# Kernel optimization log

Hardware: AMD Instinct MI355X
Metric: run time of the kernel (lower is better)

## Reference

```python
import jax, jax.numpy as jnp
import numpy as np

B, S, D_IN, D_OUT, H = 2, 2048, 1024, 1024, 16
DH = D_OUT // H

def setup_inputs() -> dict:
    key = jax.random.key(0)
    ks = jax.random.split(key, 6)
    sc = 0.02
    return {
        'x': jax.random.normal(ks[0], (B, S, D_IN), dtype=jnp.float32),
        'Wq': jax.random.normal(ks[1], (D_IN, D_OUT), dtype=jnp.float32) * sc,
        'Wk': jax.random.normal(ks[2], (D_IN, D_OUT), dtype=jnp.float32) * sc,
        'Wv': jax.random.normal(ks[3], (D_IN, D_OUT), dtype=jnp.float32) * sc,
        'Wo': jax.random.normal(ks[4], (D_OUT, D_OUT), dtype=jnp.float32) * sc,
        'bo': jax.random.normal(ks[5], (D_OUT,), dtype=jnp.float32) * sc,
    }

def reference(x, Wq, Wk, Wv, Wo, bo):
    b, s, _ = x.shape
    # projections, split heads: (b, h, s, dh)
    q = (x @ Wq).reshape(b, s, H, DH).transpose(0, 2, 1, 3)
    k = (x @ Wk).reshape(b, s, H, DH).transpose(0, 2, 1, 3)
    v = (x @ Wv).reshape(b, s, H, DH).transpose(0, 2, 1, 3)
    scores = jnp.einsum('bhqd,bhkd->bhqk', q, k)
    causal = jnp.triu(jnp.ones((s, s), dtype=bool), k=1)
    scores = jnp.where(causal, -jnp.inf, scores)
    attn = jax.nn.softmax(scores / jnp.sqrt(jnp.float32(DH)), axis=-1)
    ctx = jnp.einsum('bhqk,bhkd->bhqd', attn, v)
    ctx = ctx.transpose(0, 2, 1, 3).reshape(b, s, D_OUT)
    return ctx @ Wo + bo
```

## Files before the change

kernel.cpp:

```cpp
#include <hip/hip_runtime.h>
#include <hip/hip_bf16.h>
#include <cstdint>

typedef __attribute__((ext_vector_type(8))) __bf16 bf16x8;
typedef __attribute__((ext_vector_type(4))) float f32x4;
typedef __attribute__((ext_vector_type(8))) unsigned short u16x8;
typedef __attribute__((ext_vector_type(4))) unsigned short u16x4;
typedef __attribute__((ext_vector_type(4))) unsigned int u32x4;

#define NEG_INF (-__builtin_inff())

__device__ __forceinline__ unsigned short f2bf(float f) {
    unsigned int u = __builtin_bit_cast(unsigned int, f);
    u += 0x7FFFu + ((u >> 16) & 1u);
    return (unsigned short)(u >> 16);
}
__device__ __forceinline__ float bf2f(unsigned short u) {
    return __builtin_bit_cast(float, (unsigned int)u << 16);
}

__device__ __forceinline__ void gload16(const void* g, void* l) {
    __builtin_amdgcn_global_load_lds(
        (__attribute__((address_space(1))) void*)(uintptr_t)g,
        (__attribute__((address_space(3))) void*)(uint32_t)(uintptr_t)l, 16, 0, 0);
}

__global__ void cast_x_kernel(const float* __restrict__ x, unsigned short* __restrict__ xb) {
    size_t i = (size_t)blockIdx.x * 256 + threadIdx.x;
    const float4* p = (const float4*)x + i * 2;
    float4 a = p[0], c = p[1];
    u16x8 o;
    o[0] = f2bf(a.x); o[1] = f2bf(a.y); o[2] = f2bf(a.z); o[3] = f2bf(a.w);
    o[4] = f2bf(c.x); o[5] = f2bf(c.y); o[6] = f2bf(c.z); o[7] = f2bf(c.w);
    ((u16x8*)xb)[i] = o;
}

__global__ void castT_w_kernel(const float* __restrict__ W0, const float* __restrict__ W1,
                               const float* __restrict__ W2, const float* __restrict__ W3,
                               unsigned short* __restrict__ Wcat, unsigned short* __restrict__ Wot) {
    __shared__ float t[32][33];
    int z = blockIdx.z;
    const float* src = (z == 0) ? W0 : (z == 1) ? W1 : (z == 2) ? W2 : W3;
    unsigned short* dst = (z < 3) ? (Wcat + (size_t)z * 1024 * 1024) : Wot;
    int n0 = blockIdx.x * 32, k0 = blockIdx.y * 32;
    int tx = threadIdx.x & 31, ty = threadIdx.x >> 5;
    #pragma unroll
    for (int i = 0; i < 4; ++i) {
        int r = ty + i * 8;
        t[r][tx] = src[(size_t)(k0 + r) * 1024 + n0 + tx];
    }
    __syncthreads();
    #pragma unroll
    for (int i = 0; i < 4; ++i) {
        int r = ty + i * 8;
        dst[(size_t)(n0 + r) * 1024 + k0 + tx] = f2bf(t[tx][r]);
    }
}

__global__ __launch_bounds__(256, 2)
void gemm_qkv_kernel(const unsigned short* __restrict__ A, const unsigned short* __restrict__ Bt,
                     unsigned short* __restrict__ Qb, unsigned short* __restrict__ Kb,
                     unsigned short* __restrict__ Vtb) {
    __shared__ unsigned short As[128 * 64];
    __shared__ unsigned short Bs[128 * 64];
    const int tid = threadIdx.x;
    const int w = tid >> 6, l = tid & 63;
    const int lr = l & 15, lg = l >> 4;
    const int wr = w >> 1, wc = w & 1;
    const int m0 = blockIdx.y * 128;
    const int n0 = blockIdx.x * 128;
    const int K = 1024;

    f32x4 acc[4][4] = {};

    for (int k0 = 0; k0 < 1024; k0 += 64) {
        #pragma unroll
        for (int p = 0; p < 4; ++p) {
            int seg = p * 4 + w;
            int row = seg * 8 + (l >> 3);
            int c16 = (l & 7) ^ (row & 7);
            gload16(A  + (size_t)(m0 + row) * K + k0 + c16 * 8, &As[seg * 512]);
            gload16(Bt + (size_t)(n0 + row) * K + k0 + c16 * 8, &Bs[seg * 512]);
        }
        __syncthreads();
        #pragma unroll
        for (int ks = 0; ks < 2; ++ks) {
            bf16x8 af[4], bfr[4];
            #pragma unroll
            for (int i = 0; i < 4; ++i) {
                int ra = wr * 64 + i * 16 + lr;
                af[i] = *(const bf16x8*)&As[ra * 64 + (((ks << 2) | lg) ^ (ra & 7)) * 8];
                int rb = wc * 64 + i * 16 + lr;
                bfr[i] = *(const bf16x8*)&Bs[rb * 64 + (((ks << 2) | lg) ^ (rb & 7)) * 8];
            }
            #pragma unroll
            for (int i = 0; i < 4; ++i)
                #pragma unroll
                for (int j = 0; j < 4; ++j)
                    acc[i][j] = __builtin_amdgcn_mfma_f32_16x16x32_bf16(af[i], bfr[j], acc[i][j], 0, 0, 0);
        }
        __syncthreads();
    }

    const int seg = n0 >> 10;
    const int n0l = n0 & 1023;
    if (seg < 2) {
        unsigned short* C = (seg == 0) ? Qb : Kb;
        const float sc = (seg == 0) ? 0.125f * 1.44269504f : 1.0f;
        #pragma unroll
        for (int i = 0; i < 4; ++i)
            #pragma unroll
            for (int j = 0; j < 4; ++j) {
                int n = n0l + wc * 64 + j * 16 + lr;
                #pragma unroll
                for (int r = 0; r < 4; ++r) {
                    int m = m0 + wr * 64 + i * 16 + lg * 4 + r;
                    C[(size_t)m * 1024 + n] = f2bf(acc[i][j][r] * sc);
                }
            }
    } else {
        #pragma unroll
        for (int i = 0; i < 4; ++i)
            #pragma unroll
            for (int j = 0; j < 4; ++j) {
                int n = n0l + wc * 64 + j * 16 + lr;
                int mb = m0 + wr * 64 + i * 16 + lg * 4;
                int bb = mb >> 11, s = mb & 2047;
                int s6 = s & 63;
                int kp = (((s6 >> 4) & 1) << 5) | (((s6 >> 2) & 3) << 3) | (((s6 >> 5) & 1) << 2);
                int sp = (s & ~63) | kp;
                u16x4 o;
                #pragma unroll
                for (int r = 0; r < 4; ++r) o[r] = f2bf(acc[i][j][r]);
                *(u16x4*)&Vtb[((size_t)(bb * 1024 + n)) * 2048 + sp] = o;
            }
    }
}

static __device__ const unsigned char QS_TAB[24] = {
    7,15,15,14,14,13,13,6,12,12,11,11,5,10,10,9,9,4,8,8,3,2,1,0};
static __device__ const unsigned char TY_TAB[24] = {
    0,1,2,1,2,1,2,0,1,2,1,2,0,1,2,1,2,0,1,2,0,0,0,0};

__global__ __launch_bounds__(256, 4)
void flash_attn_kernel(const unsigned short* __restrict__ Q, const unsigned short* __restrict__ Kg,
                       const unsigned short* __restrict__ Vt, unsigned short* __restrict__ ctx,
                       unsigned short* __restrict__ P_O, float* __restrict__ P_ml) {
    __shared__ unsigned short Ks[2][4096];
    __shared__ unsigned short Vs[4096];
    const int tid = threadIdx.x, w = tid >> 6, l = tid & 63;
    const int lr = l & 15, lg = l >> 4;

    const int level = blockIdx.x >> 5;
    const int bh = blockIdx.x & 31;
    const int qs = QS_TAB[level], ty = TY_TAB[level];
    const int Tf = 2 * qs + 2, mid = qs + 1;
    const int t0 = (ty == 2) ? mid : 0;
    const int t1 = (ty == 1) ? mid : Tf;
    const int b = bh >> 4, h = bh & 15;
    const int qw = qs * 128 + w * 32;

    const int srow8 = w * 8 + (l >> 3);
    const int scol  = (l & 7) ^ (srow8 & 7);
    const unsigned short* Kbase = Kg + (size_t)(b * 2048) * 1024 + h * 64;
    const unsigned short* Vbase = Vt + (size_t)(b * 1024 + h * 64) * 2048;

    bf16x8 qf[2][2];
    #pragma unroll
    for (int mi = 0; mi < 2; ++mi)
        #pragma unroll
        for (int ks = 0; ks < 2; ++ks)
            qf[mi][ks] = *(const bf16x8*)&Q[(size_t)(b * 2048 + qw + mi * 16 + lr) * 1024 + h * 64 + ks * 32 + lg * 8];

    float mrow[2] = {NEG_INF, NEG_INF}, lrow[2] = {0.0f, 0.0f};
    f32x4 oacc[2][4] = {};

    #pragma unroll
    for (int p = 0; p < 2; ++p)
        gload16(Kbase + (size_t)(t0 * 64 + p * 32 + srow8) * 1024 + scol * 8, &Ks[0][(p * 32 + w * 8) * 64]);

    for (int t = t0; t < t1; ++t) {
        const int cur = (t - t0) & 1;
        const int k0 = t * 64;
        #pragma unroll
        for (int p = 0; p < 2; ++p)
            gload16(Vbase + (size_t)(p * 32 + srow8) * 2048 + k0 + scol * 8, &Vs[(p * 32 + w * 8) * 64]);
        const int ktn = (t + 1 < t1) ? t + 1 : t0;
        #pragma unroll
        for (int p = 0; p < 2; ++p)
            gload16(Kbase + (size_t)(ktn * 64 + p * 32 + srow8) * 1024 + scol * 8, &Ks[cur ^ 1][(p * 32 + w * 8) * 64]);

        asm volatile("s_waitcnt vmcnt(4)" ::: "memory");
        __builtin_amdgcn_s_barrier();

        f32x4 sf[2][4] = {};
        #pragma unroll
        for (int ks = 0; ks < 2; ++ks) {
            bf16x8 kf[4];
            #pragma unroll
            for (int ni = 0; ni < 4; ++ni) {
                int rk = ni * 16 + lr;
                kf[ni] = *(const bf16x8*)&Ks[cur][rk * 64 + (((ks << 2) | lg) ^ (rk & 7)) * 8];
            }
            #pragma unroll
            for (int ni = 0; ni < 4; ++ni)
                #pragma unroll
                for (int mi = 0; mi < 2; ++mi)
                    sf[mi][ni] = __builtin_amdgcn_mfma_f32_16x16x32_bf16(kf[ni], qf[mi][ks], sf[mi][ni], 0, 0, 0);
        }

        u32x4 pa0u[2], pa1u[2];
        #pragma unroll
        for (int mi = 0; mi < 2; ++mi) {
            if (t >= Tf - 2) {
                #pragma unroll
                for (int ni = 0; ni < 4; ++ni)
                    #pragma unroll
                    for (int r = 0; r < 4; ++r)
                        if (k0 + ni * 16 + lg * 4 + r > qw + mi * 16 + lr) sf[mi][ni][r] = NEG_INF;
            }
            float vmax = fmaxf(fmaxf(fmaxf(sf[mi][0][0], sf[mi][0][1]), fmaxf(sf[mi][0][2], sf[mi][0][3])),
                               fmaxf(fmaxf(sf[mi][1][0], sf[mi][1][1]), fmaxf(sf[mi][1][2], sf[mi][1][3])));
            vmax = fmaxf(vmax, fmaxf(fmaxf(fmaxf(sf[mi][2][0], sf[mi][2][1]), fmaxf(sf[mi][2][2], sf[mi][2][3])),
                                     fmaxf(fmaxf(sf[mi][3][0], sf[mi][3][1]), fmaxf(sf[mi][3][2], sf[mi][3][3]))));
            vmax = fmaxf(vmax, __shfl_xor(vmax, 16));
            vmax = fmaxf(vmax, __shfl_xor(vmax, 32));
            float mn = fmaxf(mrow[mi], vmax);
            float av = __builtin_amdgcn_exp2f(mrow[mi] - mn);
            mrow[mi] = mn;
            float rs = 0.0f;
            #pragma unroll
            for (int ni = 0; ni < 4; ++ni)
                #pragma unroll
                for (int r = 0; r < 4; ++r) {
                    float pv = __builtin_amdgcn_exp2f(sf[mi][ni][r] - mn);
                    rs += pv;
                    sf[mi][ni][r] = pv;
                }
            rs += __shfl_xor(rs, 16);
            rs += __shfl_xor(rs, 32);
            lrow[mi] = lrow[mi] * av + rs;

            asm("v_cvt_pk_bf16_f32 %0, %1, %2" : "=v"(pa0u[mi][0]) : "v"(sf[mi][0][0]), "v"(sf[mi][0][1]));
            asm("v_cvt_pk_bf16_f32 %0, %1, %2" : "=v"(pa0u[mi][1]) : "v"(sf[mi][0][2]), "v"(sf[mi][0][3]));
            asm("v_cvt_pk_bf16_f32 %0, %1, %2" : "=v"(pa0u[mi][2]) : "v"(sf[mi][2][0]), "v"(sf[mi][2][1]));
            asm("v_cvt_pk_bf16_f32 %0, %1, %2" : "=v"(pa0u[mi][3]) : "v"(sf[mi][2][2]), "v"(sf[mi][2][3]));
            asm("v_cvt_pk_bf16_f32 %0, %1, %2" : "=v"(pa1u[mi][0]) : "v"(sf[mi][1][0]), "v"(sf[mi][1][1]));
            asm("v_cvt_pk_bf16_f32 %0, %1, %2" : "=v"(pa1u[mi][1]) : "v"(sf[mi][1][2]), "v"(sf[mi][1][3]));
            asm("v_cvt_pk_bf16_f32 %0, %1, %2" : "=v"(pa1u[mi][2]) : "v"(sf[mi][3][0]), "v"(sf[mi][3][1]));
            asm("v_cvt_pk_bf16_f32 %0, %1, %2" : "=v"(pa1u[mi][3]) : "v"(sf[mi][3][2]), "v"(sf[mi][3][3]));

            float avr[4];
            #pragma unroll
            for (int r = 0; r < 4; ++r) avr[r] = __shfl(av, lg * 4 + r);
            #pragma unroll
            for (int ni = 0; ni < 4; ++ni)
                #pragma unroll
                for (int r = 0; r < 4; ++r)
                    oacc[mi][ni][r] *= avr[r];
        }

        asm volatile("s_waitcnt vmcnt(2)" ::: "memory");
        __builtin_amdgcn_s_barrier();

        #pragma unroll
        for (int ks = 0; ks < 2; ++ks) {
            bf16x8 vb[4];
            #pragma unroll
            for (int ni = 0; ni < 4; ++ni) {
                int rv = ni * 16 + lr;
                vb[ni] = *(const bf16x8*)&Vs[rv * 64 + (((ks << 2) | lg) ^ (rv & 7)) * 8];
            }
            #pragma unroll
            for (int mi = 0; mi < 2; ++mi) {
                bf16x8 pa = __builtin_bit_cast(bf16x8, ks ? pa1u[mi] : pa0u[mi]);
                #pragma unroll
                for (int ni = 0; ni < 4; ++ni)
                    oacc[mi][ni] = __builtin_amdgcn_mfma_f32_16x16x32_bf16(pa, vb[ni], oacc[mi][ni], 0, 0, 0);
            }
        }

        __builtin_amdgcn_s_barrier();
    }

    if (ty == 0) {
        #pragma unroll
        for (int mi = 0; mi < 2; ++mi) {
            float lr4[4];
            #pragma unroll
            for (int r = 0; r < 4; ++r) lr4[r] = __shfl(lrow[mi], lg * 4 + r);
            #pragma unroll
            for (int r = 0; r < 4; ++r) {
                float inv = 1.0f / lr4[r];
                int q = qw + mi * 16 + lg * 4 + r;
                size_t base = (size_t)(b * 2048 + q) * 1024 + h * 64 + lr;
                #pragma unroll
                for (int ni = 0; ni < 4; ++ni)
                    ctx[base + ni * 16] = f2bf(oacc[mi][ni][r] * inv);
            }
        }
    } else {
        const int pidx = ((qs - 8) * 32 + bh) * 2 + (ty - 1);
        unsigned short* po = P_O + (size_t)pidx * 8192;
        #pragma unroll
        for (int mi = 0; mi < 2; ++mi)
            #pragma unroll
            for (int r = 0; r < 4; ++r) {
                int rowl = w * 32 + mi * 16 + lg * 4 + r;
                #pragma unroll
                for (int ni = 0; ni < 4; ++ni)
                    po[rowl * 64 + ni * 16 + lr] = f2bf(oacc[mi][ni][r]);
            }
        if (lg == 0) {
            #pragma unroll
            for (int mi = 0; mi < 2; ++mi) {
                int rowm = w * 32 + mi * 16 + lr;
                P_ml[pidx * 256 + rowm * 2]     = mrow[mi];
                P_ml[pidx * 256 + rowm * 2 + 1] = lrow[mi];
            }
        }
    }
}

__global__ __launch_bounds__(256)
void combine_kernel(const unsigned short* __restrict__ P_O, const float* __restrict__ P_ml,
                    unsigned short* __restrict__ ctx) {
    const int qs = 8 + (blockIdx.x >> 5);
    const int bh = blockIdx.x & 31;
    const int b = bh >> 4, h = bh & 15;
    const int p0 = ((qs - 8) * 32 + bh) * 2, p1 = p0 + 1;
    const int t = threadIdx.x;
    const int row = t >> 1, half = t & 1;
    const float m0 = P_ml[p0 * 256 + row * 2], l0 = P_ml[p0 * 256 + row * 2 + 1];
    const float m1 = P_ml[p1 * 256 + row * 2], l1 = P_ml[p1 * 256 + row * 2 + 1];
    const float m = fmaxf(m0, m1);
    float f0 = __builtin_amdgcn_exp2f(m0 - m);
    float f1 = __builtin_amdgcn_exp2f(m1 - m);
    const float inv = 1.0f / (l0 * f0 + l1 * f1);
    f0 *= inv; f1 *= inv;
    const u16x8* o0 = (const u16x8*)&P_O[(size_t)p0 * 8192 + row * 64 + half * 32];
    const u16x8* o1 = (const u16x8*)&P_O[(size_t)p1 * 8192 + row * 64 + half * 32];
    unsigned short* dst = ctx + (size_t)(b * 2048 + qs * 128 + row) * 1024 + h * 64 + half * 32;
    #pragma unroll
    for (int v = 0; v < 4; ++v) {
        u16x8 a = o0[v], c = o1[v], o;
        #pragma unroll
        for (int j = 0; j < 8; ++j)
            o[j] = f2bf(bf2f(a[j]) * f0 + bf2f(c[j]) * f1);
        ((u16x8*)dst)[v] = o;
    }
}

__global__ __launch_bounds__(256, 2)
void gemm_out_kernel(const unsigned short* __restrict__ A, const unsigned short* __restrict__ Bt,
                     float* __restrict__ C, const float* __restrict__ bias) {
    __shared__ unsigned short As[128 * 64];
    __shared__ unsigned short Bs[128 * 64];
    const int tid = threadIdx.x;
    const int w = tid >> 6, l = tid & 63;
    const int lr = l & 15, lg = l >> 4;
    const int wr = w >> 1, wc = w & 1;
    const int m0 = blockIdx.y * 128;
    const int n0 = blockIdx.x * 128;
    const int K = 1024;

    f32x4 acc[4][4] = {};

    for (int k0 = 0; k0 < 1024; k0 += 64) {
        #pragma unroll
        for (int p = 0; p < 4; ++p) {
            int seg = p * 4 + w;
            int row = seg * 8 + (l >> 3);
            int c16 = (l & 7) ^ (row & 7);
            gload16(A  + (size_t)(m0 + row) * K + k0 + c16 * 8, &As[seg * 512]);
            gload16(Bt + (size_t)(n0 + row) * K + k0 + c16 * 8, &Bs[seg * 512]);
        }
        __syncthreads();
        #pragma unroll
        for (int ks = 0; ks < 2; ++ks) {
            bf16x8 af[4], bfr[4];
            #pragma unroll
            for (int i = 0; i < 4; ++i) {
                int ra = wr * 64 + i * 16 + lr;
                af[i] = *(const bf16x8*)&As[ra * 64 + (((ks << 2) | lg) ^ (ra & 7)) * 8];
                int rb = wc * 64 + i * 16 + lr;
                bfr[i] = *(const bf16x8*)&Bs[rb * 64 + (((ks << 2) | lg) ^ (rb & 7)) * 8];
            }
            #pragma unroll
            for (int i = 0; i < 4; ++i)
                #pragma unroll
                for (int j = 0; j < 4; ++j)
                    acc[i][j] = __builtin_amdgcn_mfma_f32_16x16x32_bf16(af[i], bfr[j], acc[i][j], 0, 0, 0);
        }
        __syncthreads();
    }

    #pragma unroll
    for (int i = 0; i < 4; ++i)
        #pragma unroll
        for (int j = 0; j < 4; ++j) {
            int n = n0 + wc * 64 + j * 16 + lr;
            float bv = bias[n];
            #pragma unroll
            for (int r = 0; r < 4; ++r) {
                int m = m0 + wr * 64 + i * 16 + lg * 4 + r;
                C[(size_t)m * 1024 + n] = acc[i][j][r] + bv;
            }
        }
}

extern "C" void kernel_launch(void* const* d_in, const int* in_sizes, int n_in,
                              void* d_out, int out_size, void* d_ws, size_t ws_size,
                              hipStream_t stream) {
    (void)in_sizes; (void)n_in; (void)out_size; (void)ws_size;
    const float* x  = (const float*)d_in[0];
    const float* Wq = (const float*)d_in[1];
    const float* Wk = (const float*)d_in[2];
    const float* Wv = (const float*)d_in[3];
    const float* Wo = (const float*)d_in[4];
    const float* bo = (const float*)d_in[5];
    float* out = (float*)d_out;

    char* ws = (char*)d_ws;
    const size_t MB = 1024 * 1024;
    unsigned short* xb   = (unsigned short*)(ws);
    unsigned short* Wcat = (unsigned short*)(ws + 8  * MB);
    unsigned short* Wot  = (unsigned short*)(ws + 14 * MB);
    unsigned short* Qb   = (unsigned short*)(ws + 16 * MB);
    unsigned short* Kb   = (unsigned short*)(ws + 24 * MB);
    unsigned short* Vtb  = (unsigned short*)(ws + 32 * MB);
    unsigned short* Cxb  = (unsigned short*)(ws + 40 * MB);

    unsigned short* P_O  = (unsigned short*)(ws);
    float*          P_ml = (float*)(ws + 8 * MB);

    cast_x_kernel<<<2048, 256, 0, stream>>>(x, xb);
    castT_w_kernel<<<dim3(32, 32, 4), 256, 0, stream>>>(Wq, Wk, Wv, Wo, Wcat, Wot);
    gemm_qkv_kernel<<<dim3(24, 32), 256, 0, stream>>>(xb, Wcat, Qb, Kb, Vtb);
    flash_attn_kernel<<<768, 256, 0, stream>>>(Qb, Kb, Vtb, Cxb, P_O, P_ml);
    combine_kernel<<<256, 256, 0, stream>>>(P_O, P_ml, Cxb);
    gemm_out_kernel<<<dim3(8, 32), 256, 0, stream>>>(Cxb, Wot, out, bo);
}
```

Before: 103.6 us.

## Swizzle GEMM tiles, lazy softmax rescale, MFMA row sums, double-buffer V

Both GEMMs remap block IDs with an XCD-style swizzle so neighbouring tiles share L2. The flash-attention kernel reorders its work table and double-buffers V in LDS, which lets it drop the trailing barrier. It skips the online-softmax rescale when the row max grows by at most 8 (log2 units), and computes row sums with an MFMA against a ones vector instead of shuffle reductions. The lazy rescale lets exp values reach up to 2^8 in bf16, and the new work-table order could change load balance.

```diff
diff --git a/kernel.cpp b/kernel.cpp
--- a/kernel.cpp
+++ b/kernel.cpp
@@ -67,8 +67,10 @@
     const int w = tid >> 6, l = tid & 63;
     const int lr = l & 15, lg = l >> 4;
     const int wr = w >> 1, wc = w & 1;
-    const int m0 = blockIdx.y * 128;
-    const int n0 = blockIdx.x * 128;
+    const int id = blockIdx.y * 24 + blockIdx.x;
+    const int swz = (id & 7) * 96 + (id >> 3);
+    const int m0 = (swz / 24) * 128;
+    const int n0 = (swz % 24) * 128;
     const int K = 1024;
 
     f32x4 acc[4][4] = {};
@@ -138,16 +140,20 @@
 }
 
 static __device__ const unsigned char QS_TAB[24] = {
-    7,15,15,14,14,13,13,6,12,12,11,11,5,10,10,9,9,4,8,8,3,2,1,0};
+    7,15,14,14,13,6,12,5,
+    15,13,12,10,11,10,11,9,
+    0,1,2,3,8,8,9,4};
 static __device__ const unsigned char TY_TAB[24] = {
-    0,1,2,1,2,1,2,0,1,2,1,2,0,1,2,1,2,0,1,2,0,0,0,0};
+    0,2,1,2,2,0,2,0,
+    1,1,1,1,1,2,2,2,
+    0,0,0,0,1,2,1,0};
 
 __global__ __launch_bounds__(256, 4)
 void flash_attn_kernel(const unsigned short* __restrict__ Q, const unsigned short* __restrict__ Kg,
                        const unsigned short* __restrict__ Vt, unsigned short* __restrict__ ctx,
                        unsigned short* __restrict__ P_O, float* __restrict__ P_ml) {
     __shared__ unsigned short Ks[2][4096];
-    __shared__ unsigned short Vs[4096];
+    __shared__ unsigned short Vs[2][4096];
     const int tid = threadIdx.x, w = tid >> 6, l = tid & 63;
     const int lr = l & 15, lg = l >> 4;
 
@@ -165,6 +171,9 @@
     const unsigned short* Kbase = Kg + (size_t)(b * 2048) * 1024 + h * 64;
     const unsigned short* Vbase = Vt + (size_t)(b * 1024 + h * 64) * 2048;
 
+    const __bf16 one = (__bf16)1.0f;
+    const bf16x8 ones = {one, one, one, one, one, one, one, one};
+
     bf16x8 qf[2][2];
     #pragma unroll
     for (int mi = 0; mi < 2; ++mi)
@@ -172,7 +181,8 @@
         for (int ks = 0; ks < 2; ++ks)
             qf[mi][ks] = *(const bf16x8*)&Q[(size_t)(b * 2048 + qw + mi * 16 + lr) * 1024 + h * 64 + ks * 32 + lg * 8];
 
-    float mrow[2] = {NEG_INF, NEG_INF}, lrow[2] = {0.0f, 0.0f};
+    float mrow[2] = {NEG_INF, NEG_INF};
+    f32x4 lacc[2] = {};
     f32x4 oacc[2][4] = {};
 
     #pragma unroll
@@ -184,7 +194,7 @@
         const int k0 = t * 64;
         #pragma unroll
         for (int p = 0; p < 2; ++p)
-            gload16(Vbase + (size_t)(p * 32 + srow8) * 2048 + k0 + scol * 8, &Vs[(p * 32 + w * 8) * 64]);
+            gload16(Vbase + (size_t)(p * 32 + srow8) * 2048 + k0 + scol * 8, &Vs[cur][(p * 32 + w * 8) * 64]);
         const int ktn = (t + 1 < t1) ? t + 1 : t0;
         #pragma unroll
         for (int p = 0; p < 2; ++p)
@@ -225,21 +235,26 @@
                                      fmaxf(fmaxf(sf[mi][3][0], sf[mi][3][1]), fmaxf(sf[mi][3][2], sf[mi][3][3]))));
             vmax = fmaxf(vmax, __shfl_xor(vmax, 16));
             vmax = fmaxf(vmax, __shfl_xor(vmax, 32));
-            float mn = fmaxf(mrow[mi], vmax);
-            float av = __builtin_amdgcn_exp2f(mrow[mi] - mn);
-            mrow[mi] = mn;
-            float rs = 0.0f;
+            if (!__all(vmax <= mrow[mi] + 8.0f)) {
+                float mn = fmaxf(mrow[mi], vmax);
+                float av = __builtin_amdgcn_exp2f(mrow[mi] - mn);
+                mrow[mi] = mn;
+                float avr[4];
+                #pragma unroll
+                for (int r = 0; r < 4; ++r) avr[r] = __shfl(av, lg * 4 + r);
+                #pragma unroll
+                for (int ni = 0; ni < 4; ++ni)
+                    #pragma unroll
+                    for (int r = 0; r < 4; ++r)
+                        oacc[mi][ni][r] *= avr[r];
+                #pragma unroll
+                for (int r = 0; r < 4; ++r) lacc[mi][r] *= avr[r];
+            }
             #pragma unroll
             for (int ni = 0; ni < 4; ++ni)
                 #pragma unroll
-                for (int r = 0; r < 4; ++r) {
-                    float pv = __builtin_amdgcn_exp2f(sf[mi][ni][r] - mn);
-                    rs += pv;
-                    sf[mi][ni][r] = pv;
-                }
-            rs += __shfl_xor(rs, 16);
-            rs += __shfl_xor(rs, 32);
-            lrow[mi] = lrow[mi] * av + rs;
+                for (int r = 0; r < 4; ++r)
+                    sf[mi][ni][r] = __builtin_amdgcn_exp2f(sf[mi][ni][r] - mrow[mi]);
 
             asm("v_cvt_pk_bf16_f32 %0, %1, %2" : "=v"(pa0u[mi][0]) : "v"(sf[mi][0][0]), "v"(sf[mi][0][1]));
             asm("v_cvt_pk_bf16_f32 %0, %1, %2" : "=v"(pa0u[mi][1]) : "v"(sf[mi][0][2]), "v"(sf[mi][0][3]));
@@ -250,14 +265,10 @@
             asm("v_cvt_pk_bf16_f32 %0, %1, %2" : "=v"(pa1u[mi][2]) : "v"(sf[mi][3][0]), "v"(sf[mi][3][1]));
             asm("v_cvt_pk_bf16_f32 %0, %1, %2" : "=v"(pa1u[mi][3]) : "v"(sf[mi][3][2]), "v"(sf[mi][3][3]));
 
-            float avr[4];
-            #pragma unroll
-            for (int r = 0; r < 4; ++r) avr[r] = __shfl(av, lg * 4 + r);
-            #pragma unroll
-            for (int ni = 0; ni < 4; ++ni)
-                #pragma unroll
-                for (int r = 0; r < 4; ++r)
-                    oacc[mi][ni][r] *= avr[r];
+            lacc[mi] = __builtin_amdgcn_mfma_f32_16x16x32_bf16(
+                __builtin_bit_cast(bf16x8, pa0u[mi]), ones, lacc[mi], 0, 0, 0);
+            lacc[mi] = __builtin_amdgcn_mfma_f32_16x16x32_bf16(
+                __builtin_bit_cast(bf16x8, pa1u[mi]), ones, lacc[mi], 0, 0, 0);
         }
 
         asm volatile("s_waitcnt vmcnt(2)" ::: "memory");
@@ -269,7 +280,7 @@
             #pragma unroll
             for (int ni = 0; ni < 4; ++ni) {
                 int rv = ni * 16 + lr;
-                vb[ni] = *(const bf16x8*)&Vs[rv * 64 + (((ks << 2) | lg) ^ (rv & 7)) * 8];
+                vb[ni] = *(const bf16x8*)&Vs[cur][rv * 64 + (((ks << 2) | lg) ^ (rv & 7)) * 8];
             }
             #pragma unroll
             for (int mi = 0; mi < 2; ++mi) {
@@ -279,26 +290,20 @@
                     oacc[mi][ni] = __builtin_amdgcn_mfma_f32_16x16x32_bf16(pa, vb[ni], oacc[mi][ni], 0, 0, 0);
             }
         }
-
-        __builtin_amdgcn_s_barrier();
     }
 
     if (ty == 0) {
         #pragma unroll
-        for (int mi = 0; mi < 2; ++mi) {
-            float lr4[4];
-            #pragma unroll
-            for (int r = 0; r < 4; ++r) lr4[r] = __shfl(lrow[mi], lg * 4 + r);
+        for (int mi = 0; mi < 2; ++mi)
             #pragma unroll
             for (int r = 0; r < 4; ++r) {
-                float inv = 1.0f / lr4[r];
+                float inv = 1.0f / lacc[mi][r];
                 int q = qw + mi * 16 + lg * 4 + r;
                 size_t base = (size_t)(b * 2048 + q) * 1024 + h * 64 + lr;
                 #pragma unroll
                 for (int ni = 0; ni < 4; ++ni)
                     ctx[base + ni * 16] = f2bf(oacc[mi][ni][r] * inv);
             }
-        }
     } else {
         const int pidx = ((qs - 8) * 32 + bh) * 2 + (ty - 1);
         unsigned short* po = P_O + (size_t)pidx * 8192;
@@ -313,11 +318,15 @@
             }
         if (lg == 0) {
             #pragma unroll
-            for (int mi = 0; mi < 2; ++mi) {
-                int rowm = w * 32 + mi * 16 + lr;
-                P_ml[pidx * 256 + rowm * 2]     = mrow[mi];
-                P_ml[pidx * 256 + rowm * 2 + 1] = lrow[mi];
-            }
+            for (int mi = 0; mi < 2; ++mi)
+                P_ml[pidx * 256 + (w * 32 + mi * 16 + lr) * 2] = mrow[mi];
+        }
+        if (lr == 0) {
+            #pragma unroll
+            for (int mi = 0; mi < 2; ++mi)
+                #pragma unroll
+                for (int r = 0; r < 4; ++r)
+                    P_ml[pidx * 256 + (w * 32 + mi * 16 + lg * 4 + r) * 2 + 1] = lacc[mi][r];
         }
     }
 }
@@ -360,8 +369,10 @@
     const int w = tid >> 6, l = tid & 63;
     const int lr = l & 15, lg = l >> 4;
     const int wr = w >> 1, wc = w & 1;
-    const int m0 = blockIdx.y * 128;
-    const int n0 = blockIdx.x * 128;
+    const int id = blockIdx.y * 8 + blockIdx.x;
+    const int swz = (id & 7) * 32 + (id >> 3);
+    const int m0 = (swz / 8) * 128;
+    const int n0 = (swz % 8) * 128;
     const int K = 1024;
 
     f32x4 acc[4][4] = {};
```

After: 97.84 us. 5.6% less time.
